# Optimization experiments

Hardware: AMD Instinct MI355X
Metric: run time of the kernel (lower is better)

Reference implementation:

```python
import jax, jax.numpy as jnp
import numpy as np

N = 50000   # nodes
E = 1000000 # edges
D = 64      # input_nf = output_nf = hidden_nf
COORDS_WEIGHT = 1.0


def setup_inputs() -> dict:
    key = jax.random.key(0)
    ks = jax.random.split(key, 16)
    h = jax.random.normal(ks[0], (N, D), dtype=jnp.float32)
    coord = jax.random.normal(ks[1], (N, 3), dtype=jnp.float32)
    edge_index = jax.random.randint(ks[2], (2, E), 0, N, dtype=jnp.int32)
    s = 0.05  # generic init scale
    # edge_mlp: Linear(2D+1 -> D), ReLU, Linear(D -> D), ReLU
    We1 = jax.random.normal(ks[3], (2 * D + 1, D), dtype=jnp.float32) * s
    be1 = jnp.zeros((D,), dtype=jnp.float32)
    We2 = jax.random.normal(ks[4], (D, D), dtype=jnp.float32) * s
    be2 = jnp.zeros((D,), dtype=jnp.float32)
    # node_mlp: Linear(2D -> D), ReLU, Linear(D -> D)
    Wn1 = jax.random.normal(ks[5], (2 * D, D), dtype=jnp.float32) * s
    bn1 = jnp.zeros((D,), dtype=jnp.float32)
    Wn2 = jax.random.normal(ks[6], (D, D), dtype=jnp.float32) * s
    bn2 = jnp.zeros((D,), dtype=jnp.float32)
    # coord_mlp: Linear(D -> D), ReLU, Linear(D -> 1, no bias, xavier gain 0.001)
    Wc1 = jax.random.normal(ks[7], (D, D), dtype=jnp.float32) * s
    bc1 = jnp.zeros((D,), dtype=jnp.float32)
    Wc2 = jax.random.normal(ks[8], (D, 1), dtype=jnp.float32) * 0.001
    return {"h": h, "coord": coord, "edge_index": edge_index,
            "We1": We1, "be1": be1, "We2": We2, "be2": be2,
            "Wn1": Wn1, "bn1": bn1, "Wn2": Wn2, "bn2": bn2,
            "Wc1": Wc1, "bc1": bc1, "Wc2": Wc2}


def reference(h, coord, edge_index, We1, be1, We2, be2, Wn1, bn1, Wn2, bn2, Wc1, bc1, Wc2):
    row, col = edge_index[0], edge_index[1]
    # coord2radial (no PBC offsets; plain pairwise difference)
    coord_diff = coord[row] - coord[col]                    # [E, 3]
    radial = jnp.sum(coord_diff ** 2, axis=1, keepdims=True)  # [E, 1]

    # edge model: MLP on [h_i, h_j, ||x_i - x_j||^2]
    e_in = jnp.concatenate([h[row], h[col], radial], axis=1)  # [E, 2D+1]
    m = jax.nn.relu(e_in @ We1 + be1)
    edge_feat = jax.nn.relu(m @ We2 + be2)                   # [E, D]

    # coord model: per-edge scalar gate, clamp, segment mean
    gate = jax.nn.relu(edge_feat @ Wc1 + bc1) @ Wc2          # [E, 1]
    trans = jnp.clip(coord_diff * gate, -100.0, 100.0)       # [E, 3]
    trans_sum = jax.ops.segment_sum(trans, row, num_segments=N)  # [N, 3]
    cnt = jax.ops.segment_sum(jnp.ones((row.shape[0],), dtype=trans.dtype), row, num_segments=N)
    coord_out = (trans_sum / jnp.maximum(cnt, 1.0)[:, None]) * COORDS_WEIGHT  # [N, 3]

    # node model: scatter-sum aggregate then MLP with residual
    agg = jax.ops.segment_sum(edge_feat, row, num_segments=N)  # [N, D]
    n_in = jnp.concatenate([h, agg], axis=1)                   # [N, 2D]
    h_out = h + (jax.nn.relu(n_in @ Wn1 + bn1) @ Wn2 + bn2)    # residual
    return (h_out, coord_out)
```

## Files before the change

kernel.cpp:

```cpp
#include <hip/hip_runtime.h>

typedef float  f32x4  __attribute__((ext_vector_type(4)));
typedef __bf16 bf16x8 __attribute__((ext_vector_type(8)));
typedef unsigned short u16x8 __attribute__((ext_vector_type(8)));

__device__ inline unsigned short f2b(float f) {
    unsigned u = __builtin_bit_cast(unsigned, f);
    u += 0x7fffu + ((u >> 16) & 1u);
    return (unsigned short)(u >> 16);
}

__device__ inline f32x4 mfma16(bf16x8 a, bf16x8 b, f32x4 c) {
    return __builtin_amdgcn_mfma_f32_16x16x32_bf16(a, b, c, 0, 0, 0);
}

__device__ inline bf16x8 cvt8(f32x4 a, f32x4 b) {
    u16x8 v;
    v[0] = f2b(a[0]); v[1] = f2b(a[1]); v[2] = f2b(a[2]); v[3] = f2b(a[3]);
    v[4] = f2b(b[0]); v[5] = f2b(b[1]); v[6] = f2b(b[2]); v[7] = f2b(b[3]);
    return __builtin_bit_cast(bf16x8, v);
}

__device__ inline bf16x8 ldsA(const unsigned short* base, int frag, int lane) {
    return __builtin_bit_cast(bf16x8,
        *reinterpret_cast<const u16x8*>(base + ((frag * 64 + lane) << 3)));
}

__device__ inline void atom_pk(unsigned short* p, unsigned d) {
    asm volatile("global_atomic_pk_add_bf16 %0, %1, off" :: "v"(p), "v"(d) : "memory");
}

template<bool PK>
__global__ __launch_bounds__(512, 4) void egcl_edge(
    const float* __restrict__ h, const unsigned short* __restrict__ hb,
    const float* __restrict__ coord,
    const int* __restrict__ erow, const int* __restrict__ ecol,
    const float* __restrict__ We1, const float* __restrict__ be1,
    const float* __restrict__ We2, const float* __restrict__ be2,
    const float* __restrict__ Wc1, const float* __restrict__ bc1,
    const float* __restrict__ Wc2,
    float* __restrict__ aggf, unsigned short* __restrict__ aggb,
    float* __restrict__ cacc, int E)
{
    __shared__ __align__(16) unsigned short A1[16 * 512];
    __shared__ __align__(16) unsigned short A2[8 * 512];
    __shared__ __align__(16) unsigned short A3[8 * 512];
    __shared__ __align__(16) float bv[5][64];
    __shared__ __align__(16) unsigned stl[8][16 * 33];

    const int t = threadIdx.x;
    for (int i = t; i < 8192; i += 512) {
        int j = i & 7, lane = (i >> 3) & 63, fi = i >> 9;
        int mt = fi >> 2, ks = fi & 3;
        int in_ch = ks * 32 + ((lane >> 4) << 3) + j;
        int out   = mt * 16 + (lane & 15);
        A1[i] = f2b(We1[in_ch * 64 + out]);
    }
    for (int i = t; i < 4096; i += 512) {
        int j = i & 7, lane = (i >> 3) & 63, fi = i >> 9;
        int mt = fi >> 1, ks = fi & 1;
        int c   = (ks * 2 + (j >> 2)) * 16 + ((lane >> 4) & 3) * 4 + (j & 3);
        int out = mt * 16 + (lane & 15);
        A2[i] = f2b(We2[c * 64 + out]);
        A3[i] = f2b(Wc1[c * 64 + out]);
    }
    if (t < 64) {
        bv[0][t] = be1[t]; bv[1][t] = We1[128 * 64 + t];
        bv[2][t] = be2[t]; bv[3][t] = bc1[t]; bv[4][t] = Wc2[t];
    }
    __syncthreads();

    const int lane = t & 63;
    const int l16 = lane & 15, lq = lane >> 4;
    const int stride = gridDim.x * 8;
    const int wid = (blockIdx.x << 3) + (t >> 6);
    const int ntile = E >> 4;
    const int last = ntile - 1;
    unsigned* st = stl[t >> 6];

    int tile = wid;
    if (tile >= ntile) return;

    if constexpr (PK) {
        int eC = (tile << 4) + l16;
        int rC = erow[eC], cC = ecol[eC];
        u16x8 hr0, hr1, hc0, hc1;
        {
            const u16x8* hr = reinterpret_cast<const u16x8*>(hb + (size_t)rC * 64);
            const u16x8* hc = reinterpret_cast<const u16x8*>(hb + (size_t)cC * 64);
            hr0 = hr[lq]; hr1 = hr[4 + lq]; hc0 = hc[lq]; hc1 = hc[4 + lq];
        }
        float px = 0.f, py = 0.f, pz = 0.f;
        if (lq < 2) {
            int node = (lq == 0) ? rC : cC;
            const float* pp = coord + (size_t)node * 3;
            px = pp[0]; py = pp[1]; pz = pp[2];
        }
        int t1 = tile + stride;
        int tn = (t1 < ntile) ? t1 : last;
        int eN = (tn << 4) + l16;
        int rN = erow[eN], cN = ecol[eN];

        for (; tile < ntile; ) {
            u16x8 nr0, nr1, nc0, nc1;
            {
                const u16x8* hr = reinterpret_cast<const u16x8*>(hb + (size_t)rN * 64);
                const u16x8* hc = reinterpret_cast<const u16x8*>(hb + (size_t)cN * 64);
                nr0 = hr[lq]; nr1 = hr[4 + lq]; nc0 = hc[lq]; nc1 = hc[4 + lq];
            }
            float npx = 0.f, npy = 0.f, npz = 0.f;
            if (lq < 2) {
                int node = (lq == 0) ? rN : cN;
                const float* pp = coord + (size_t)node * 3;
                npx = pp[0]; npy = pp[1]; npz = pp[2];
            }
            int t2 = tile + 2 * stride;
            int t2c = (t2 < ntile) ? t2 : last;
            int e2 = (t2c << 4) + l16;
            int rNN = erow[e2], cNN = ecol[e2];

            float prx = __shfl(px, l16, 64), pry = __shfl(py, l16, 64), prz = __shfl(pz, l16, 64);
            float pcx = __shfl(px, 16 + l16, 64), pcy = __shfl(py, 16 + l16, 64), pcz = __shfl(pz, 16 + l16, 64);
            float dx = prx - pcx, dy = pry - pcy, dz = prz - pcz;
            float rad = dx * dx + dy * dy + dz * dz;

            bf16x8 bR[2] = { __builtin_bit_cast(bf16x8, hr0), __builtin_bit_cast(bf16x8, hr1) };
            bf16x8 bC[2] = { __builtin_bit_cast(bf16x8, hc0), __builtin_bit_cast(bf16x8, hc1) };

            f32x4 a1[4];
#pragma unroll
            for (int mt = 0; mt < 4; ++mt)
                a1[mt] = *reinterpret_cast<const f32x4*>(&bv[0][mt * 16 + lq * 4]);
#pragma unroll
            for (int ks = 0; ks < 2; ++ks)
#pragma unroll
                for (int mt = 0; mt < 4; ++mt)
                    a1[mt] = mfma16(ldsA(A1, mt * 4 + ks, lane), bR[ks], a1[mt]);
#pragma unroll
            for (int ks = 0; ks < 2; ++ks)
#pragma unroll
                for (int mt = 0; mt < 4; ++mt)
                    a1[mt] = mfma16(ldsA(A1, mt * 4 + 2 + ks, lane), bC[ks], a1[mt]);
#pragma unroll
            for (int mt = 0; mt < 4; ++mt) {
                f32x4 w = *reinterpret_cast<const f32x4*>(&bv[1][mt * 16 + lq * 4]);
#pragma unroll
                for (int rr = 0; rr < 4; ++rr)
                    a1[mt][rr] = fmaxf(a1[mt][rr] + rad * w[rr], 0.f);
            }

            bf16x8 b2[2] = { cvt8(a1[0], a1[1]), cvt8(a1[2], a1[3]) };
            f32x4 a2[4];
#pragma unroll
            for (int mt = 0; mt < 4; ++mt)
                a2[mt] = *reinterpret_cast<const f32x4*>(&bv[2][mt * 16 + lq * 4]);
#pragma unroll
            for (int ks = 0; ks < 2; ++ks)
#pragma unroll
                for (int mt = 0; mt < 4; ++mt)
                    a2[mt] = mfma16(ldsA(A2, mt * 2 + ks, lane), b2[ks], a2[mt]);
#pragma unroll
            for (int mt = 0; mt < 4; ++mt)
#pragma unroll
                for (int rr = 0; rr < 4; ++rr)
                    a2[mt][rr] = fmaxf(a2[mt][rr], 0.f);

#pragma unroll
            for (int mt = 0; mt < 4; ++mt) {
                unsigned w0 = (unsigned)f2b(a2[mt][0]) | ((unsigned)f2b(a2[mt][1]) << 16);
                unsigned w1 = (unsigned)f2b(a2[mt][2]) | ((unsigned)f2b(a2[mt][3]) << 16);
                st[l16 * 33 + mt * 8 + lq * 2 + 0] = w0;
                st[l16 * 33 + mt * 8 + lq * 2 + 1] = w1;
            }

            bf16x8 b3[2] = { cvt8(a2[0], a2[1]), cvt8(a2[2], a2[3]) };
            f32x4 a3[4];
#pragma unroll
            for (int mt = 0; mt < 4; ++mt)
                a3[mt] = *reinterpret_cast<const f32x4*>(&bv[3][mt * 16 + lq * 4]);
#pragma unroll
            for (int ks = 0; ks < 2; ++ks)
#pragma unroll
                for (int mt = 0; mt < 4; ++mt)
                    a3[mt] = mfma16(ldsA(A3, mt * 2 + ks, lane), b3[ks], a3[mt]);
            float g = 0.f;
#pragma unroll
            for (int mt = 0; mt < 4; ++mt) {
                f32x4 w = *reinterpret_cast<const f32x4*>(&bv[4][mt * 16 + lq * 4]);
#pragma unroll
                for (int rr = 0; rr < 4; ++rr)
                    g += fmaxf(a3[mt][rr], 0.f) * w[rr];
            }
            g += __shfl_xor(g, 16, 64);
            g += __shfl_xor(g, 32, 64);

#pragma unroll
            for (int i = 0; i < 8; ++i) {
                int e  = (i << 1) | (lane >> 5);
                int cp = ((lane >> 4) & 1) * 16 + (lane & 15);
                unsigned pkd = st[e * 33 + cp];
                int rw = __shfl(rC, e, 64);
                atom_pk(aggb + (size_t)rw * 64 + cp * 2, pkd);
            }

            float dsel = (lq == 0) ? dx : (lq == 1) ? dy : dz;
            float val  = (lq == 3) ? 1.0f : fminf(fmaxf(dsel * g, -100.f), 100.f);
            atomicAdd(&cacc[(size_t)rC * 4 + lq], val);

            tile = t1; t1 = tile + stride;
            rC = rN; cC = cN; rN = rNN; cN = cNN;
            hr0 = nr0; hr1 = nr1; hc0 = nc0; hc1 = nc1;
            px = npx; py = npy; pz = npz;
        }
    } else {
        for (; tile < ntile; tile += stride) {
            const int e = (tile << 4) + l16;
            const int r = erow[e], c = ecol[e];
            const float* pr = coord + (size_t)r * 3;
            const float* pc = coord + (size_t)c * 3;
            float dx = pr[0] - pc[0], dy = pr[1] - pc[1], dz = pr[2] - pc[2];
            float rad = dx * dx + dy * dy + dz * dz;
            const f32x4* hr = reinterpret_cast<const f32x4*>(h + (size_t)r * 64);
            const f32x4* hc = reinterpret_cast<const f32x4*>(h + (size_t)c * 64);
            bf16x8 bR[2], bC[2];
#pragma unroll
            for (int ks = 0; ks < 2; ++ks) {
                bR[ks] = cvt8(hr[ks * 8 + lq * 2], hr[ks * 8 + lq * 2 + 1]);
                bC[ks] = cvt8(hc[ks * 8 + lq * 2], hc[ks * 8 + lq * 2 + 1]);
            }
            f32x4 a1[4];
#pragma unroll
            for (int mt = 0; mt < 4; ++mt)
                a1[mt] = *reinterpret_cast<const f32x4*>(&bv[0][mt * 16 + lq * 4]);
#pragma unroll
            for (int ks = 0; ks < 2; ++ks)
#pragma unroll
                for (int mt = 0; mt < 4; ++mt)
                    a1[mt] = mfma16(ldsA(A1, mt * 4 + ks, lane), bR[ks], a1[mt]);
#pragma unroll
            for (int ks = 0; ks < 2; ++ks)
#pragma unroll
                for (int mt = 0; mt < 4; ++mt)
                    a1[mt] = mfma16(ldsA(A1, mt * 4 + 2 + ks, lane), bC[ks], a1[mt]);
#pragma unroll
            for (int mt = 0; mt < 4; ++mt) {
                f32x4 w = *reinterpret_cast<const f32x4*>(&bv[1][mt * 16 + lq * 4]);
#pragma unroll
                for (int rr = 0; rr < 4; ++rr)
                    a1[mt][rr] = fmaxf(a1[mt][rr] + rad * w[rr], 0.f);
            }
            bf16x8 b2[2] = { cvt8(a1[0], a1[1]), cvt8(a1[2], a1[3]) };
            f32x4 a2[4];
#pragma unroll
            for (int mt = 0; mt < 4; ++mt)
                a2[mt] = *reinterpret_cast<const f32x4*>(&bv[2][mt * 16 + lq * 4]);
#pragma unroll
            for (int ks = 0; ks < 2; ++ks)
#pragma unroll
                for (int mt = 0; mt < 4; ++mt)
                    a2[mt] = mfma16(ldsA(A2, mt * 2 + ks, lane), b2[ks], a2[mt]);
#pragma unroll
            for (int mt = 0; mt < 4; ++mt)
#pragma unroll
                for (int rr = 0; rr < 4; ++rr) {
                    a2[mt][rr] = fmaxf(a2[mt][rr], 0.f);
                    atomicAdd(&aggf[(size_t)r * 64 + mt * 16 + lq * 4 + rr], a2[mt][rr]);
                }
            bf16x8 b3[2] = { cvt8(a2[0], a2[1]), cvt8(a2[2], a2[3]) };
            f32x4 a3[4];
#pragma unroll
            for (int mt = 0; mt < 4; ++mt)
                a3[mt] = *reinterpret_cast<const f32x4*>(&bv[3][mt * 16 + lq * 4]);
#pragma unroll
            for (int ks = 0; ks < 2; ++ks)
#pragma unroll
                for (int mt = 0; mt < 4; ++mt)
                    a3[mt] = mfma16(ldsA(A3, mt * 2 + ks, lane), b3[ks], a3[mt]);
            float g = 0.f;
#pragma unroll
            for (int mt = 0; mt < 4; ++mt) {
                f32x4 w = *reinterpret_cast<const f32x4*>(&bv[4][mt * 16 + lq * 4]);
#pragma unroll
                for (int rr = 0; rr < 4; ++rr)
                    g += fmaxf(a3[mt][rr], 0.f) * w[rr];
            }
            g += __shfl_xor(g, 16, 64);
            g += __shfl_xor(g, 32, 64);
            float dsel = (lq == 0) ? dx : (lq == 1) ? dy : dz;
            float val  = (lq == 3) ? 1.0f : fminf(fmaxf(dsel * g, -100.f), 100.f);
            atomicAdd(&cacc[(size_t)r * 4 + lq], val);
        }
    }
}

__device__ inline void stage_wblock(unsigned short* dst, const float* src, int t, int nthr) {
    for (int i = t; i < 4096; i += nthr) {
        int k = i >> 6, n = i & 63;
        int pos = (((n >> 4) * 2 + (k >> 5)) * 64 + ((((k >> 3) & 3) << 4) | (n & 15))) * 8 + (k & 7);
        dst[pos] = f2b(src[i]);
    }
}

__device__ inline bf16x8 ldsB(const unsigned short* base, int nt, int ks, int lane) {
    return __builtin_bit_cast(bf16x8,
        *reinterpret_cast<const u16x8*>(base + (((nt * 2 + ks) * 64 + lane) << 3)));
}

template<bool PK>
__global__ __launch_bounds__(256) void egcl_node(
    const float* __restrict__ h, const unsigned short* __restrict__ hb,
    const float* __restrict__ aggf, const unsigned short* __restrict__ aggb,
    const float* __restrict__ Wn1, const float* __restrict__ bn1,
    const float* __restrict__ Wn2, const float* __restrict__ bn2,
    float* __restrict__ hout, int N)
{
    __shared__ __align__(16) unsigned short wlds[3][4096];
    __shared__ __align__(16) unsigned short mlds[4][16 * 72];
    __shared__ float bn1l[64], bn2l[64];

    const int t = threadIdx.x;
    stage_wblock(wlds[0], Wn1, t, 256);
    stage_wblock(wlds[1], Wn1 + 64 * 64, t, 256);
    stage_wblock(wlds[2], Wn2, t, 256);
    if (t < 64) { bn1l[t] = bn1[t]; bn2l[t] = bn2[t]; }
    __syncthreads();

    const int wave = t >> 6, lane = t & 63;
    const int l16 = lane & 15, lq = lane >> 4;
    const int ntile = N >> 4;
    unsigned short* ml = mlds[wave];

    for (int tile = blockIdx.x * 4 + wave; tile < ntile; tile += gridDim.x * 4) {
        const int nb = tile << 4;
        bf16x8 fH[2], fA[2];
        if constexpr (PK) {
            const u16x8* ph = reinterpret_cast<const u16x8*>(hb + (size_t)(nb + l16) * 64);
            const u16x8* pa = reinterpret_cast<const u16x8*>(aggb + (size_t)(nb + l16) * 64);
#pragma unroll
            for (int ks = 0; ks < 2; ++ks) {
                fH[ks] = __builtin_bit_cast(bf16x8, ph[ks * 4 + lq]);
                fA[ks] = __builtin_bit_cast(bf16x8, pa[ks * 4 + lq]);
            }
        } else {
            const f32x4* ph = reinterpret_cast<const f32x4*>(h + (size_t)(nb + l16) * 64);
            const f32x4* pa = reinterpret_cast<const f32x4*>(aggf + (size_t)(nb + l16) * 64);
#pragma unroll
            for (int ks = 0; ks < 2; ++ks) {
                fH[ks] = cvt8(ph[ks * 8 + lq * 2], ph[ks * 8 + lq * 2 + 1]);
                fA[ks] = cvt8(pa[ks * 8 + lq * 2], pa[ks * 8 + lq * 2 + 1]);
            }
        }
        f32x4 acc[4];
#pragma unroll
        for (int nt = 0; nt < 4; ++nt) { float b = bn1l[nt * 16 + l16]; acc[nt] = (f32x4){b, b, b, b}; }
#pragma unroll
        for (int ks = 0; ks < 2; ++ks)
#pragma unroll
            for (int nt = 0; nt < 4; ++nt)
                acc[nt] = mfma16(fH[ks], ldsB(wlds[0], nt, ks, lane), acc[nt]);
#pragma unroll
        for (int ks = 0; ks < 2; ++ks)
#pragma unroll
            for (int nt = 0; nt < 4; ++nt)
                acc[nt] = mfma16(fA[ks], ldsB(wlds[1], nt, ks, lane), acc[nt]);
#pragma unroll
        for (int nt = 0; nt < 4; ++nt)
#pragma unroll
            for (int r = 0; r < 4; ++r)
                ml[(lq * 4 + r) * 72 + nt * 16 + l16] = f2b(fmaxf(acc[nt][r], 0.f));
        bf16x8 fM[2];
#pragma unroll
        for (int ks = 0; ks < 2; ++ks)
            fM[ks] = __builtin_bit_cast(bf16x8,
                *reinterpret_cast<const u16x8*>(ml + l16 * 72 + ks * 32 + lq * 8));
        f32x4 acc2[4];
#pragma unroll
        for (int nt = 0; nt < 4; ++nt) { float b = bn2l[nt * 16 + l16]; acc2[nt] = (f32x4){b, b, b, b}; }
#pragma unroll
        for (int ks = 0; ks < 2; ++ks)
#pragma unroll
            for (int nt = 0; nt < 4; ++nt)
                acc2[nt] = mfma16(fM[ks], ldsB(wlds[2], nt, ks, lane), acc2[nt]);
#pragma unroll
        for (int nt = 0; nt < 4; ++nt)
#pragma unroll
            for (int r = 0; r < 4; ++r) {
                size_t idx = (size_t)(nb + lq * 4 + r) * 64 + nt * 16 + l16;
                hout[idx] = h[idx] + acc2[nt][r];
            }
    }
}

__global__ void f32_to_bf16(const float* __restrict__ src, unsigned short* __restrict__ dst, int n8)
{
    int i = blockIdx.x * 256 + threadIdx.x;
    if (i < n8) {
        const f32x4* p = reinterpret_cast<const f32x4*>(src + (size_t)i * 8);
        bf16x8 v = cvt8(p[0], p[1]);
        reinterpret_cast<u16x8*>(dst)[i] = __builtin_bit_cast(u16x8, v);
    }
}

__global__ void egcl_coord(const float* __restrict__ cacc, float* __restrict__ cout, int N)
{
    int n = blockIdx.x * 256 + threadIdx.x;
    if (n < N) {
        f32x4 c = *reinterpret_cast<const f32x4*>(cacc + (size_t)n * 4);
        float inv = 1.f / fmaxf(c[3], 1.f);
        cout[n * 3 + 0] = c[0] * inv;
        cout[n * 3 + 1] = c[1] * inv;
        cout[n * 3 + 2] = c[2] * inv;
    }
}

extern "C" void kernel_launch(void* const* d_in, const int* in_sizes, int n_in,
                              void* d_out, int out_size, void* d_ws, size_t ws_size,
                              hipStream_t stream)
{
    const float* h     = (const float*)d_in[0];
    const float* coord = (const float*)d_in[1];
    const int*   eidx  = (const int*)d_in[2];
    const float* We1 = (const float*)d_in[3];  const float* be1 = (const float*)d_in[4];
    const float* We2 = (const float*)d_in[5];  const float* be2 = (const float*)d_in[6];
    const float* Wn1 = (const float*)d_in[7];  const float* bn1 = (const float*)d_in[8];
    const float* Wn2 = (const float*)d_in[9];  const float* bn2 = (const float*)d_in[10];
    const float* Wc1 = (const float*)d_in[11]; const float* bc1 = (const float*)d_in[12];
    const float* Wc2 = (const float*)d_in[13];

    const int N = in_sizes[0] / 64;
    const int E = in_sizes[2] / 2;

    float* hout = (float*)d_out;
    float* cout = hout + (size_t)N * 64;

    float*          cacc = (float*)d_ws;
    unsigned short* aggb = (unsigned short*)((char*)d_ws + (1u << 20));
    unsigned short* hb   = (unsigned short*)((char*)d_ws + (8u << 20));
    const size_t need = (8u << 20) + (size_t)N * 64 * 2;
    const bool pk = (ws_size >= need);

    hipMemsetAsync(cacc, 0, (size_t)N * 4 * sizeof(float), stream);

    const int ntileN = N >> 4;
    const int nblkN  = (ntileN + 3) / 4;

    if (pk) {
        hipMemsetAsync(aggb, 0, (size_t)N * 64 * 2, stream);
        int n8 = N * 8;
        f32_to_bf16<<<(n8 + 255) / 256, 256, 0, stream>>>(h, hb, n8);
        egcl_edge<true><<<2048, 512, 0, stream>>>(h, hb, coord, eidx, eidx + E,
                                                  We1, be1, We2, be2, Wc1, bc1, Wc2,
                                                  nullptr, aggb, cacc, E);
        egcl_node<true><<<nblkN, 256, 0, stream>>>(h, hb, nullptr, aggb,
                                                   Wn1, bn1, Wn2, bn2, hout, N);
    } else {
        float* aggf = hout;
        hipMemsetAsync(aggf, 0, (size_t)N * 64 * sizeof(float), stream);
        egcl_edge<false><<<2048, 512, 0, stream>>>(h, nullptr, coord, eidx, eidx + E,
                                                   We1, be1, We2, be2, Wc1, bc1, Wc2,
                                                   aggf, nullptr, cacc, E);
        egcl_node<false><<<nblkN, 256, 0, stream>>>(h, nullptr, aggf, nullptr,
                                                    Wn1, bn1, Wn2, bn2, hout, N);
    }
    egcl_coord<<<(N + 255) / 256, 256, 0, stream>>>(cacc, cout, N);
}
```

Before: 203.8 us.

## Sort edges by row into CSR and aggregate per node without atomics

Each call now builds a CSR layout from the edge rows with a histogram, a single-block scan and an atomic scatter. The edge MLP then runs per group of 8 destination nodes, reading the row features once from LDS. Edge messages and coordinate updates are reduced serially within the wave and written directly, which removes the packed bf16 and fp32 global atomics, the memsets and the separate coord-normalisation kernel. In exchange it adds three preprocessing kernels with their own atomics, a serial per-edge flush loop with shuffles, and load imbalance when node degrees vary.

```diff
diff --git a/kernel.cpp b/kernel.cpp
--- a/kernel.cpp
+++ b/kernel.cpp
@@ -26,27 +26,77 @@
         *reinterpret_cast<const u16x8*>(base + ((frag * 64 + lane) << 3)));
 }
 
-__device__ inline void atom_pk(unsigned short* p, unsigned d) {
-    asm volatile("global_atomic_pk_add_bf16 %0, %1, off" :: "v"(p), "v"(d) : "memory");
-}
-
-template<bool PK>
-__global__ __launch_bounds__(512, 4) void egcl_edge(
-    const float* __restrict__ h, const unsigned short* __restrict__ hb,
+__global__ void k_hist(const int* __restrict__ erow, int* __restrict__ cnt, int E)
+{
+    int i = blockIdx.x * 256 + threadIdx.x;
+    if (i < E) atomicAdd(&cnt[erow[i]], 1);
+}
+
+__global__ void k_scan(const int* __restrict__ cnt, int* __restrict__ off,
+                       int* __restrict__ woff, int N, int E)
+{
+    __shared__ int wsum[16];
+    const int t = threadIdx.x;
+    const int lane = t & 63, w = t >> 6;
+    const int chunk = (N + 1023) >> 10;
+    const int lo = t * chunk;
+    const int hi = (lo + chunk < N) ? lo + chunk : N;
+    int s = 0;
+    for (int i = lo; i < hi; ++i) s += cnt[i];
+    int sc = s;
+#pragma unroll
+    for (int d = 1; d < 64; d <<= 1) {
+        int v = __shfl_up(sc, d, 64);
+        if (lane >= d) sc += v;
+    }
+    if (lane == 63) wsum[w] = sc;
+    __syncthreads();
+    if (w == 0 && lane < 16) {
+        int v = wsum[lane];
+        int scw = v;
+#pragma unroll
+        for (int d = 1; d < 16; d <<= 1) {
+            int u = __shfl_up(scw, d, 16);
+            if (lane >= d) scw += u;
+        }
+        wsum[lane] = scw - v;
+    }
+    __syncthreads();
+    int run = wsum[w] + (sc - s);
+    for (int i = lo; i < hi; ++i) {
+        off[i] = run; woff[i] = run;
+        run += cnt[i];
+    }
+    if (t == 0) off[N] = E;
+}
+
+__global__ void k_scatter(const int* __restrict__ erow, const int* __restrict__ ecol,
+                          int* __restrict__ woff, int* __restrict__ scol, int E)
+{
+    int i = blockIdx.x * 256 + threadIdx.x;
+    if (i < E) {
+        int pos = atomicAdd(&woff[erow[i]], 1);
+        scol[pos] = ecol[i];
+    }
+}
+
+__global__ __launch_bounds__(512, 4) void egcl_edge_sorted(
+    const unsigned short* __restrict__ hb,
     const float* __restrict__ coord,
-    const int* __restrict__ erow, const int* __restrict__ ecol,
+    const int* __restrict__ off, const int* __restrict__ scol,
     const float* __restrict__ We1, const float* __restrict__ be1,
     const float* __restrict__ We2, const float* __restrict__ be2,
     const float* __restrict__ Wc1, const float* __restrict__ bc1,
     const float* __restrict__ Wc2,
-    float* __restrict__ aggf, unsigned short* __restrict__ aggb,
-    float* __restrict__ cacc, int E)
+    float* __restrict__ aggf, float* __restrict__ cout, int N)
 {
     __shared__ __align__(16) unsigned short A1[16 * 512];
     __shared__ __align__(16) unsigned short A2[8 * 512];
     __shared__ __align__(16) unsigned short A3[8 * 512];
     __shared__ __align__(16) float bv[5][64];
     __shared__ __align__(16) unsigned stl[8][16 * 33];
+    __shared__ __align__(16) unsigned short hl[8][8 * 72];
+    __shared__ __align__(16) float cl[8][32];
 
     const int t = threadIdx.x;
     for (int i = t; i < 8192; i += 512) {
@@ -72,224 +122,313 @@
 
     const int lane = t & 63;
     const int l16 = lane & 15, lq = lane >> 4;
+    const int w = t >> 6;
+    unsigned* st = stl[w];
+    unsigned short* hrw = hl[w];
+    float* crw = cl[w];
+
+    const int nT = N >> 3;
+    const int tile = blockIdx.x * 8 + w;
+    if (tile >= nT) return;
+    const int nb = tile << 3;
+
+    {
+        int row = lane >> 3, ck = lane & 7;
+        *reinterpret_cast<u16x8*>(hrw + row * 72 + ck * 8) =
+            *reinterpret_cast<const u16x8*>(hb + (size_t)(nb + row) * 64 + ck * 8);
+    }
+    if (lane < 32) {
+        int nn = lane >> 2, c4 = lane & 3;
+        crw[lane] = (c4 < 3) ? coord[(size_t)(nb + nn) * 3 + c4] : 0.f;
+    }
+
+    int ok[9];
+#pragma unroll
+    for (int k = 0; k < 9; ++k) ok[k] = off[nb + k];
+    const int s0 = ok[0], s1 = ok[8];
+    const int dd0 = ok[1]-ok[0], dd1 = ok[2]-ok[1], dd2 = ok[3]-ok[2], dd3 = ok[4]-ok[3];
+    const int dd4 = ok[5]-ok[4], dd5 = ok[6]-ok[5], dd6 = ok[7]-ok[6], dd7 = ok[8]-ok[7];
+
+    int cur = -1; float accv = 0.f, caccv = 0.f;
+    auto FLUSH = [&]() {
+        if (cur >= 0) {
+            aggf[(size_t)(nb + cur) * 64 + lane] = accv;
+            if (lane < 3) {
+                int cc = cur==0?dd0:cur==1?dd1:cur==2?dd2:cur==3?dd3:
+                         cur==4?dd4:cur==5?dd5:cur==6?dd6:dd7;
+                cout[(size_t)(nb + cur) * 3 + lane] = caccv * (1.f / fmaxf((float)cc, 1.f));
+            }
+        }
+    };
+
+    const int nE = s1 - s0;
+    if (nE > 0) {
+        const int s1m1 = s1 - 1;
+        const int nG = (nE + 15) >> 4;
+
+        int gb = s0;
+        int p  = gb + l16;
+        {
+            int pm = (p < s1m1) ? p : s1m1;
+            int c0 = scol[pm];
+            const u16x8* hp = reinterpret_cast<const u16x8*>(hb + (size_t)c0 * 64);
+            u16x8 h0 = hp[lq], h1 = hp[4 + lq];
+            float cx = 0.f, cy = 0.f, cz = 0.f;
+            if (lq == 1) { const float* pp = coord + (size_t)c0 * 3; cx = pp[0]; cy = pp[1]; cz = pp[2]; }
+            int q1 = gb + 16 + l16;
+            int c1 = scol[(q1 < s1m1) ? q1 : s1m1];
+
+            u16x8 hc0 = h0, hc1 = h1;
+            float cpx = cx, cpy = cy, cpz = cz;
+
+            for (int g = 0; g < nG; ++g) {
+                u16x8 nh0, nh1;
+                {
+                    const u16x8* np = reinterpret_cast<const u16x8*>(hb + (size_t)c1 * 64);
+                    nh0 = np[lq]; nh1 = np[4 + lq];
+                }
+                float nx = 0.f, ny = 0.f, nz = 0.f;
+                if (lq == 1) { const float* pp = coord + (size_t)c1 * 3; nx = pp[0]; ny = pp[1]; nz = pp[2]; }
+                int q2 = gb + 32 + l16;
+                int c2 = scol[(q2 < s1m1) ? q2 : s1m1];
+
+                int ni = 0;
+#pragma unroll
+                for (int k = 1; k < 8; ++k) ni += (p >= ok[k]) ? 1 : 0;
+
+                bf16x8 bR[2];
+                bR[0] = __builtin_bit_cast(bf16x8,
+                        *reinterpret_cast<const u16x8*>(hrw + ni * 72 + lq * 8));
+                bR[1] = __builtin_bit_cast(bf16x8,
+                        *reinterpret_cast<const u16x8*>(hrw + ni * 72 + (4 + lq) * 8));
+                bf16x8 bC[2] = { __builtin_bit_cast(bf16x8, hc0), __builtin_bit_cast(bf16x8, hc1) };
+
+                float prx = crw[ni * 4 + 0], pry = crw[ni * 4 + 1], prz = crw[ni * 4 + 2];
+                float pcx = __shfl(cpx, 16 + l16, 64);
+                float pcy = __shfl(cpy, 16 + l16, 64);
+                float pcz = __shfl(cpz, 16 + l16, 64);
+                float dx = prx - pcx, dy = pry - pcy, dz = prz - pcz;
+                float rad = dx * dx + dy * dy + dz * dz;
+
+                f32x4 a1[4];
+#pragma unroll
+                for (int mt = 0; mt < 4; ++mt)
+                    a1[mt] = *reinterpret_cast<const f32x4*>(&bv[0][mt * 16 + lq * 4]);
+#pragma unroll
+                for (int ks = 0; ks < 2; ++ks)
+#pragma unroll
+                    for (int mt = 0; mt < 4; ++mt)
+                        a1[mt] = mfma16(ldsA(A1, mt * 4 + ks, lane), bR[ks], a1[mt]);
+#pragma unroll
+                for (int ks = 0; ks < 2; ++ks)
+#pragma unroll
+                    for (int mt = 0; mt < 4; ++mt)
+                        a1[mt] = mfma16(ldsA(A1, mt * 4 + 2 + ks, lane), bC[ks], a1[mt]);
+#pragma unroll
+                for (int mt = 0; mt < 4; ++mt) {
+                    f32x4 wv = *reinterpret_cast<const f32x4*>(&bv[1][mt * 16 + lq * 4]);
+#pragma unroll
+                    for (int rr = 0; rr < 4; ++rr)
+                        a1[mt][rr] = fmaxf(a1[mt][rr] + rad * wv[rr], 0.f);
+                }
+
+                bf16x8 b2[2] = { cvt8(a1[0], a1[1]), cvt8(a1[2], a1[3]) };
+                f32x4 a2[4];
+#pragma unroll
+                for (int mt = 0; mt < 4; ++mt)
+                    a2[mt] = *reinterpret_cast<const f32x4*>(&bv[2][mt * 16 + lq * 4]);
+#pragma unroll
+                for (int ks = 0; ks < 2; ++ks)
+#pragma unroll
+                    for (int mt = 0; mt < 4; ++mt)
+                        a2[mt] = mfma16(ldsA(A2, mt * 2 + ks, lane), b2[ks], a2[mt]);
+#pragma unroll
+                for (int mt = 0; mt < 4; ++mt)
+#pragma unroll
+                    for (int rr = 0; rr < 4; ++rr)
+                        a2[mt][rr] = fmaxf(a2[mt][rr], 0.f);
+
+#pragma unroll
+                for (int mt = 0; mt < 4; ++mt) {
+                    unsigned w0 = (unsigned)f2b(a2[mt][0]) | ((unsigned)f2b(a2[mt][1]) << 16);
+                    unsigned w1 = (unsigned)f2b(a2[mt][2]) | ((unsigned)f2b(a2[mt][3]) << 16);
+                    st[l16 * 33 + mt * 8 + lq * 2 + 0] = w0;
+                    st[l16 * 33 + mt * 8 + lq * 2 + 1] = w1;
+                }
+
+                bf16x8 b3[2] = { cvt8(a2[0], a2[1]), cvt8(a2[2], a2[3]) };
+                f32x4 a3[4];
+#pragma unroll
+                for (int mt = 0; mt < 4; ++mt)
+                    a3[mt] = *reinterpret_cast<const f32x4*>(&bv[3][mt * 16 + lq * 4]);
+#pragma unroll
+                for (int ks = 0; ks < 2; ++ks)
+#pragma unroll
+                    for (int mt = 0; mt < 4; ++mt)
+                        a3[mt] = mfma16(ldsA(A3, mt * 2 + ks, lane), b3[ks], a3[mt]);
+                float gg = 0.f;
+#pragma unroll
+                for (int mt = 0; mt < 4; ++mt) {
+                    f32x4 wv = *reinterpret_cast<const f32x4*>(&bv[4][mt * 16 + lq * 4]);
+#pragma unroll
+                    for (int rr = 0; rr < 4; ++rr)
+                        gg += fmaxf(a3[mt][rr], 0.f) * wv[rr];
+                }
+                gg += __shfl_xor(gg, 16, 64);
+                gg += __shfl_xor(gg, 32, 64);
+
+                float dsel = (lq == 0) ? dx : (lq == 1) ? dy : dz;
+                float val  = fminf(fmaxf(dsel * gg, -100.f), 100.f);
+
+#pragma unroll
+                for (int e = 0; e < 16; ++e) {
+                    if (gb + e < s1) {
+                        int nv = __shfl(ni, e, 64);
+                        unsigned wrd = st[e * 33 + (lane >> 1)];
+                        float v = __builtin_bit_cast(float,
+                                  (lane & 1) ? (wrd & 0xffff0000u) : (wrd << 16));
+                        float cv = __shfl(val, ((lane & 3) << 4) + e, 64);
+                        if (nv != cur) { FLUSH(); cur = nv; accv = v; caccv = cv; }
+                        else           { accv += v; caccv += cv; }
+                    }
+                }
+
+                gb += 16; p += 16;
+                c1 = c2;
+                hc0 = nh0; hc1 = nh1;
+                cpx = nx; cpy = ny; cpz = nz;
+            }
+        }
+        FLUSH();
+    }
+
+#pragma unroll
+    for (int k = 0; k < 8; ++k) {
+        if (ok[k + 1] == ok[k]) {
+            aggf[(size_t)(nb + k) * 64 + lane] = 0.f;
+            if (lane < 3) cout[(size_t)(nb + k) * 3 + lane] = 0.f;
+        }
+    }
+}
+
+__global__ __launch_bounds__(512, 4) void egcl_edge_fb(
+    const float* __restrict__ h, const float* __restrict__ coord,
+    const int* __restrict__ erow, const int* __restrict__ ecol,
+    const float* __restrict__ We1, const float* __restrict__ be1,
+    const float* __restrict__ We2, const float* __restrict__ be2,
+    const float* __restrict__ Wc1, const float* __restrict__ bc1,
+    const float* __restrict__ Wc2,
+    float* __restrict__ aggf, float* __restrict__ cacc, int E)
+{
+    __shared__ __align__(16) unsigned short A1[16 * 512];
+    __shared__ __align__(16) unsigned short A2[8 * 512];
+    __shared__ __align__(16) unsigned short A3[8 * 512];
+    __shared__ __align__(16) float bv[5][64];
+
+    const int t = threadIdx.x;
+    for (int i = t; i < 8192; i += 512) {
+        int j = i & 7, lane = (i >> 3) & 63, fi = i >> 9;
+        int mt = fi >> 2, ks = fi & 3;
+        int in_ch = ks * 32 + ((lane >> 4) << 3) + j;
+        int out   = mt * 16 + (lane & 15);
+        A1[i] = f2b(We1[in_ch * 64 + out]);
+    }
+    for (int i = t; i < 4096; i += 512) {
+        int j = i & 7, lane = (i >> 3) & 63, fi = i >> 9;
+        int mt = fi >> 1, ks = fi & 1;
+        int c   = (ks * 2 + (j >> 2)) * 16 + ((lane >> 4) & 3) * 4 + (j & 3);
+        int out = mt * 16 + (lane & 15);
+        A2[i] = f2b(We2[c * 64 + out]);
+        A3[i] = f2b(Wc1[c * 64 + out]);
+    }
+    if (t < 64) {
+        bv[0][t] = be1[t]; bv[1][t] = We1[128 * 64 + t];
+        bv[2][t] = be2[t]; bv[3][t] = bc1[t]; bv[4][t] = Wc2[t];
+    }
+    __syncthreads();
+
+    const int lane = t & 63;
+    const int l16 = lane & 15, lq = lane >> 4;
     const int stride = gridDim.x * 8;
     const int wid = (blockIdx.x << 3) + (t >> 6);
     const int ntile = E >> 4;
-    const int last = ntile - 1;
-    unsigned* st = stl[t >> 6];
-
-    int tile = wid;
-    if (tile >= ntile) return;
-
-    if constexpr (PK) {
-        int eC = (tile << 4) + l16;
-        int rC = erow[eC], cC = ecol[eC];
-        u16x8 hr0, hr1, hc0, hc1;
-        {
-            const u16x8* hr = reinterpret_cast<const u16x8*>(hb + (size_t)rC * 64);
-            const u16x8* hc = reinterpret_cast<const u16x8*>(hb + (size_t)cC * 64);
-            hr0 = hr[lq]; hr1 = hr[4 + lq]; hc0 = hc[lq]; hc1 = hc[4 + lq];
-        }
-        float px = 0.f, py = 0.f, pz = 0.f;
-        if (lq < 2) {
-            int node = (lq == 0) ? rC : cC;
-            const float* pp = coord + (size_t)node * 3;
-            px = pp[0]; py = pp[1]; pz = pp[2];
-        }
-        int t1 = tile + stride;
-        int tn = (t1 < ntile) ? t1 : last;
-        int eN = (tn << 4) + l16;
-        int rN = erow[eN], cN = ecol[eN];
-
-        for (; tile < ntile; ) {
-            u16x8 nr0, nr1, nc0, nc1;
-            {
-                const u16x8* hr = reinterpret_cast<const u16x8*>(hb + (size_t)rN * 64);
-                const u16x8* hc = reinterpret_cast<const u16x8*>(hb + (size_t)cN * 64);
-                nr0 = hr[lq]; nr1 = hr[4 + lq]; nc0 = hc[lq]; nc1 = hc[4 + lq];
+
+    for (int tile = wid; tile < ntile; tile += stride) {
+        const int e = (tile << 4) + l16;
+        const int r = erow[e], c = ecol[e];
+        const float* pr = coord + (size_t)r * 3;
+        const float* pc = coord + (size_t)c * 3;
+        float dx = pr[0] - pc[0], dy = pr[1] - pc[1], dz = pr[2] - pc[2];
+        float rad = dx * dx + dy * dy + dz * dz;
+        const f32x4* hr = reinterpret_cast<const f32x4*>(h + (size_t)r * 64);
+        const f32x4* hc = reinterpret_cast<const f32x4*>(h + (size_t)c * 64);
+        bf16x8 bR[2], bC[2];
+#pragma unroll
+        for (int ks = 0; ks < 2; ++ks) {
+            bR[ks] = cvt8(hr[ks * 8 + lq * 2], hr[ks * 8 + lq * 2 + 1]);
+            bC[ks] = cvt8(hc[ks * 8 + lq * 2], hc[ks * 8 + lq * 2 + 1]);
+        }
+        f32x4 a1[4];
+#pragma unroll
+        for (int mt = 0; mt < 4; ++mt)
+            a1[mt] = *reinterpret_cast<const f32x4*>(&bv[0][mt * 16 + lq * 4]);
+#pragma unroll
+        for (int ks = 0; ks < 2; ++ks)
+#pragma unroll
+            for (int mt = 0; mt < 4; ++mt)
+                a1[mt] = mfma16(ldsA(A1, mt * 4 + ks, lane), bR[ks], a1[mt]);
+#pragma unroll
+        for (int ks = 0; ks < 2; ++ks)
+#pragma unroll
+            for (int mt = 0; mt < 4; ++mt)
+                a1[mt] = mfma16(ldsA(A1, mt * 4 + 2 + ks, lane), bC[ks], a1[mt]);
+#pragma unroll
+        for (int mt = 0; mt < 4; ++mt) {
+            f32x4 wv = *reinterpret_cast<const f32x4*>(&bv[1][mt * 16 + lq * 4]);
+#pragma unroll
+            for (int rr = 0; rr < 4; ++rr)
+                a1[mt][rr] = fmaxf(a1[mt][rr] + rad * wv[rr], 0.f);
+        }
+        bf16x8 b2[2] = { cvt8(a1[0], a1[1]), cvt8(a1[2], a1[3]) };
+        f32x4 a2[4];
+#pragma unroll
+        for (int mt = 0; mt < 4; ++mt)
+            a2[mt] = *reinterpret_cast<const f32x4*>(&bv[2][mt * 16 + lq * 4]);
+#pragma unroll
+        for (int ks = 0; ks < 2; ++ks)
+#pragma unroll
+            for (int mt = 0; mt < 4; ++mt)
+                a2[mt] = mfma16(ldsA(A2, mt * 2 + ks, lane), b2[ks], a2[mt]);
+#pragma unroll
+        for (int mt = 0; mt < 4; ++mt)
+#pragma unroll
+            for (int rr = 0; rr < 4; ++rr) {
+                a2[mt][rr] = fmaxf(a2[mt][rr], 0.f);
+                atomicAdd(&aggf[(size_t)r * 64 + mt * 16 + lq * 4 + rr], a2[mt][rr]);
             }
-            float npx = 0.f, npy = 0.f, npz = 0.f;
-            if (lq < 2) {
-                int node = (lq == 0) ? rN : cN;
-                const float* pp = coord + (size_t)node * 3;
-                npx = pp[0]; npy = pp[1]; npz = pp[2];
-            }
-            int t2 = tile + 2 * stride;
-            int t2c = (t2 < ntile) ? t2 : last;
-            int e2 = (t2c << 4) + l16;
-            int rNN = erow[e2], cNN = ecol[e2];
-
-            float prx = __shfl(px, l16, 64), pry = __shfl(py, l16, 64), prz = __shfl(pz, l16, 64);
-            float pcx = __shfl(px, 16 + l16, 64), pcy = __shfl(py, 16 + l16, 64), pcz = __shfl(pz, 16 + l16, 64);
-            float dx = prx - pcx, dy = pry - pcy, dz = prz - pcz;
-            float rad = dx * dx + dy * dy + dz * dz;
-
-            bf16x8 bR[2] = { __builtin_bit_cast(bf16x8, hr0), __builtin_bit_cast(bf16x8, hr1) };
-            bf16x8 bC[2] = { __builtin_bit_cast(bf16x8, hc0), __builtin_bit_cast(bf16x8, hc1) };
-
-            f32x4 a1[4];
+        bf16x8 b3[2] = { cvt8(a2[0], a2[1]), cvt8(a2[2], a2[3]) };
+        f32x4 a3[4];
+#pragma unroll
+        for (int mt = 0; mt < 4; ++mt)
+            a3[mt] = *reinterpret_cast<const f32x4*>(&bv[3][mt * 16 + lq * 4]);
+#pragma unroll
+        for (int ks = 0; ks < 2; ++ks)
 #pragma unroll
             for (int mt = 0; mt < 4; ++mt)
-                a1[mt] = *reinterpret_cast<const f32x4*>(&bv[0][mt * 16 + lq * 4]);
-#pragma unroll
-            for (int ks = 0; ks < 2; ++ks)
-#pragma unroll
-                for (int mt = 0; mt < 4; ++mt)
-                    a1[mt] = mfma16(ldsA(A1, mt * 4 + ks, lane), bR[ks], a1[mt]);
-#pragma unroll
-            for (int ks = 0; ks < 2; ++ks)
-#pragma unroll
-                for (int mt = 0; mt < 4; ++mt)
-                    a1[mt] = mfma16(ldsA(A1, mt * 4 + 2 + ks, lane), bC[ks], a1[mt]);
-#pragma unroll
-            for (int mt = 0; mt < 4; ++mt) {
-                f32x4 w = *reinterpret_cast<const f32x4*>(&bv[1][mt * 16 + lq * 4]);
-#pragma unroll
-                for (int rr = 0; rr < 4; ++rr)
-                    a1[mt][rr] = fmaxf(a1[mt][rr] + rad * w[rr], 0.f);
-            }
-
-            bf16x8 b2[2] = { cvt8(a1[0], a1[1]), cvt8(a1[2], a1[3]) };
-            f32x4 a2[4];
-#pragma unroll
-            for (int mt = 0; mt < 4; ++mt)
-                a2[mt] = *reinterpret_cast<const f32x4*>(&bv[2][mt * 16 + lq * 4]);
-#pragma unroll
-            for (int ks = 0; ks < 2; ++ks)
-#pragma unroll
-                for (int mt = 0; mt < 4; ++mt)
-                    a2[mt] = mfma16(ldsA(A2, mt * 2 + ks, lane), b2[ks], a2[mt]);
-#pragma unroll
-            for (int mt = 0; mt < 4; ++mt)
-#pragma unroll
-                for (int rr = 0; rr < 4; ++rr)
-                    a2[mt][rr] = fmaxf(a2[mt][rr], 0.f);
-
-#pragma unroll
-            for (int mt = 0; mt < 4; ++mt) {
-                unsigned w0 = (unsigned)f2b(a2[mt][0]) | ((unsigned)f2b(a2[mt][1]) << 16);
-                unsigned w1 = (unsigned)f2b(a2[mt][2]) | ((unsigned)f2b(a2[mt][3]) << 16);
-                st[l16 * 33 + mt * 8 + lq * 2 + 0] = w0;
-                st[l16 * 33 + mt * 8 + lq * 2 + 1] = w1;
-            }
-
-            bf16x8 b3[2] = { cvt8(a2[0], a2[1]), cvt8(a2[2], a2[3]) };
-            f32x4 a3[4];
-#pragma unroll
-            for (int mt = 0; mt < 4; ++mt)
-                a3[mt] = *reinterpret_cast<const f32x4*>(&bv[3][mt * 16 + lq * 4]);
-#pragma unroll
-            for (int ks = 0; ks < 2; ++ks)
-#pragma unroll
-                for (int mt = 0; mt < 4; ++mt)
-                    a3[mt] = mfma16(ldsA(A3, mt * 2 + ks, lane), b3[ks], a3[mt]);
-            float g = 0.f;
-#pragma unroll
-            for (int mt = 0; mt < 4; ++mt) {
-                f32x4 w = *reinterpret_cast<const f32x4*>(&bv[4][mt * 16 + lq * 4]);
-#pragma unroll
-                for (int rr = 0; rr < 4; ++rr)
-                    g += fmaxf(a3[mt][rr], 0.f) * w[rr];
-            }
-            g += __shfl_xor(g, 16, 64);
-            g += __shfl_xor(g, 32, 64);
-
-#pragma unroll
-            for (int i = 0; i < 8; ++i) {
-                int e  = (i << 1) | (lane >> 5);
-                int cp = ((lane >> 4) & 1) * 16 + (lane & 15);
-                unsigned pkd = st[e * 33 + cp];
-                int rw = __shfl(rC, e, 64);
-                atom_pk(aggb + (size_t)rw * 64 + cp * 2, pkd);
-            }
-
-            float dsel = (lq == 0) ? dx : (lq == 1) ? dy : dz;
-            float val  = (lq == 3) ? 1.0f : fminf(fmaxf(dsel * g, -100.f), 100.f);
-            atomicAdd(&cacc[(size_t)rC * 4 + lq], val);
-
-            tile = t1; t1 = tile + stride;
-            rC = rN; cC = cN; rN = rNN; cN = cNN;
-            hr0 = nr0; hr1 = nr1; hc0 = nc0; hc1 = nc1;
-            px = npx; py = npy; pz = npz;
-        }
-    } else {
-        for (; tile < ntile; tile += stride) {
-            const int e = (tile << 4) + l16;
-            const int r = erow[e], c = ecol[e];
-            const float* pr = coord + (size_t)r * 3;
-            const float* pc = coord + (size_t)c * 3;
-            float dx = pr[0] - pc[0], dy = pr[1] - pc[1], dz = pr[2] - pc[2];
-            float rad = dx * dx + dy * dy + dz * dz;
-            const f32x4* hr = reinterpret_cast<const f32x4*>(h + (size_t)r * 64);
-            const f32x4* hc = reinterpret_cast<const f32x4*>(h + (size_t)c * 64);
-            bf16x8 bR[2], bC[2];
-#pragma unroll
-            for (int ks = 0; ks < 2; ++ks) {
-                bR[ks] = cvt8(hr[ks * 8 + lq * 2], hr[ks * 8 + lq * 2 + 1]);
-                bC[ks] = cvt8(hc[ks * 8 + lq * 2], hc[ks * 8 + lq * 2 + 1]);
-            }
-            f32x4 a1[4];
-#pragma unroll
-            for (int mt = 0; mt < 4; ++mt)
-                a1[mt] = *reinterpret_cast<const f32x4*>(&bv[0][mt * 16 + lq * 4]);
-#pragma unroll
-            for (int ks = 0; ks < 2; ++ks)
-#pragma unroll
-                for (int mt = 0; mt < 4; ++mt)
-                    a1[mt] = mfma16(ldsA(A1, mt * 4 + ks, lane), bR[ks], a1[mt]);
-#pragma unroll
-            for (int ks = 0; ks < 2; ++ks)
-#pragma unroll
-                for (int mt = 0; mt < 4; ++mt)
-                    a1[mt] = mfma16(ldsA(A1, mt * 4 + 2 + ks, lane), bC[ks], a1[mt]);
-#pragma unroll
-            for (int mt = 0; mt < 4; ++mt) {
-                f32x4 w = *reinterpret_cast<const f32x4*>(&bv[1][mt * 16 + lq * 4]);
-#pragma unroll
-                for (int rr = 0; rr < 4; ++rr)
-                    a1[mt][rr] = fmaxf(a1[mt][rr] + rad * w[rr], 0.f);
-            }
-            bf16x8 b2[2] = { cvt8(a1[0], a1[1]), cvt8(a1[2], a1[3]) };
-            f32x4 a2[4];
-#pragma unroll
-            for (int mt = 0; mt < 4; ++mt)
-                a2[mt] = *reinterpret_cast<const f32x4*>(&bv[2][mt * 16 + lq * 4]);
-#pragma unroll
-            for (int ks = 0; ks < 2; ++ks)
-#pragma unroll
-                for (int mt = 0; mt < 4; ++mt)
-                    a2[mt] = mfma16(ldsA(A2, mt * 2 + ks, lane), b2[ks], a2[mt]);
-#pragma unroll
-            for (int mt = 0; mt < 4; ++mt)
-#pragma unroll
-                for (int rr = 0; rr < 4; ++rr) {
-                    a2[mt][rr] = fmaxf(a2[mt][rr], 0.f);
-                    atomicAdd(&aggf[(size_t)r * 64 + mt * 16 + lq * 4 + rr], a2[mt][rr]);
-                }
-            bf16x8 b3[2] = { cvt8(a2[0], a2[1]), cvt8(a2[2], a2[3]) };
-            f32x4 a3[4];
-#pragma unroll
-            for (int mt = 0; mt < 4; ++mt)
-                a3[mt] = *reinterpret_cast<const f32x4*>(&bv[3][mt * 16 + lq * 4]);
-#pragma unroll
-            for (int ks = 0; ks < 2; ++ks)
-#pragma unroll
-                for (int mt = 0; mt < 4; ++mt)
-                    a3[mt] = mfma16(ldsA(A3, mt * 2 + ks, lane), b3[ks], a3[mt]);
-            float g = 0.f;
-#pragma unroll
-            for (int mt = 0; mt < 4; ++mt) {
-                f32x4 w = *reinterpret_cast<const f32x4*>(&bv[4][mt * 16 + lq * 4]);
-#pragma unroll
-                for (int rr = 0; rr < 4; ++rr)
-                    g += fmaxf(a3[mt][rr], 0.f) * w[rr];
-            }
-            g += __shfl_xor(g, 16, 64);
-            g += __shfl_xor(g, 32, 64);
-            float dsel = (lq == 0) ? dx : (lq == 1) ? dy : dz;
-            float val  = (lq == 3) ? 1.0f : fminf(fmaxf(dsel * g, -100.f), 100.f);
-            atomicAdd(&cacc[(size_t)r * 4 + lq], val);
-        }
+                a3[mt] = mfma16(ldsA(A3, mt * 2 + ks, lane), b3[ks], a3[mt]);
+        float gg = 0.f;
+#pragma unroll
+        for (int mt = 0; mt < 4; ++mt) {
+            f32x4 wv = *reinterpret_cast<const f32x4*>(&bv[4][mt * 16 + lq * 4]);
+#pragma unroll
+            for (int rr = 0; rr < 4; ++rr)
+                gg += fmaxf(a3[mt][rr], 0.f) * wv[rr];
+        }
+        gg += __shfl_xor(gg, 16, 64);
+        gg += __shfl_xor(gg, 32, 64);
+        float dsel = (lq == 0) ? dx : (lq == 1) ? dy : dz;
+        float val  = (lq == 3) ? 1.0f : fminf(fmaxf(dsel * gg, -100.f), 100.f);
+        atomicAdd(&cacc[(size_t)r * 4 + lq], val);
     }
 }
 
@@ -306,10 +445,8 @@
         *reinterpret_cast<const u16x8*>(base + (((nt * 2 + ks) * 64 + lane) << 3)));
 }
 
-template<bool PK>
-__global__ __launch_bounds__(256) void egcl_node(
-    const float* __restrict__ h, const unsigned short* __restrict__ hb,
-    const float* __restrict__ aggf, const unsigned short* __restrict__ aggb,
+__global__ __launch_bounds__(256) void egcl_node_fb(
+    const float* __restrict__ h, const float* __restrict__ aggf,
     const float* __restrict__ Wn1, const float* __restrict__ bn1,
     const float* __restrict__ Wn2, const float* __restrict__ bn2,
     float* __restrict__ hout, int N)
@@ -333,22 +470,12 @@
     for (int tile = blockIdx.x * 4 + wave; tile < ntile; tile += gridDim.x * 4) {
         const int nb = tile << 4;
         bf16x8 fH[2], fA[2];
-        if constexpr (PK) {
-            const u16x8* ph = reinterpret_cast<const u16x8*>(hb + (size_t)(nb + l16) * 64);
-            const u16x8* pa = reinterpret_cast<const u16x8*>(aggb + (size_t)(nb + l16) * 64);
-#pragma unroll
-            for (int ks = 0; ks < 2; ++ks) {
-                fH[ks] = __builtin_bit_cast(bf16x8, ph[ks * 4 + lq]);
-                fA[ks] = __builtin_bit_cast(bf16x8, pa[ks * 4 + lq]);
-            }
-        } else {
-            const f32x4* ph = reinterpret_cast<const f32x4*>(h + (size_t)(nb + l16) * 64);
-            const f32x4* pa = reinterpret_cast<const f32x4*>(aggf + (size_t)(nb + l16) * 64);
-#pragma unroll
-            for (int ks = 0; ks < 2; ++ks) {
-                fH[ks] = cvt8(ph[ks * 8 + lq * 2], ph[ks * 8 + lq * 2 + 1]);
-                fA[ks] = cvt8(pa[ks * 8 + lq * 2], pa[ks * 8 + lq * 2 + 1]);
-            }
+        const f32x4* ph = reinterpret_cast<const f32x4*>(h + (size_t)(nb + l16) * 64);
+        const f32x4* pa = reinterpret_cast<const f32x4*>(aggf + (size_t)(nb + l16) * 64);
+#pragma unroll
+        for (int ks = 0; ks < 2; ++ks) {
+            fH[ks] = cvt8(ph[ks * 8 + lq * 2], ph[ks * 8 + lq * 2 + 1]);
+            fA[ks] = cvt8(pa[ks * 8 + lq * 2], pa[ks * 8 + lq * 2 + 1]);
         }
         f32x4 acc[4];
 #pragma unroll
@@ -433,34 +560,41 @@
     float* hout = (float*)d_out;
     float* cout = hout + (size_t)N * 64;
 
-    float*          cacc = (float*)d_ws;
-    unsigned short* aggb = (unsigned short*)((char*)d_ws + (1u << 20));
-    unsigned short* hb   = (unsigned short*)((char*)d_ws + (8u << 20));
-    const size_t need = (8u << 20) + (size_t)N * 64 * 2;
-    const bool pk = (ws_size >= need);
-
-    hipMemsetAsync(cacc, 0, (size_t)N * 4 * sizeof(float), stream);
-
     const int ntileN = N >> 4;
     const int nblkN  = (ntileN + 3) / 4;
 
-    if (pk) {
-        hipMemsetAsync(aggb, 0, (size_t)N * 64 * 2, stream);
+    int* cnt  = (int*)d_ws;
+    int* off  = (int*)((char*)d_ws + (256u << 10));
+    int* woff = (int*)((char*)d_ws + (512u << 10));
+    int* scol = (int*)((char*)d_ws + (1u << 20));
+    unsigned short* hb = (unsigned short*)((char*)d_ws + (5u << 20));
+
+    const size_t need_sorted = (5u << 20) + (size_t)N * 128;
+    const bool use_sorted = (ws_size >= need_sorted) && (N % 16 == 0) && N > 0
+                            && ((size_t)E * 4 <= (4u << 20));
+
+    if (use_sorted) {
+        hipMemsetAsync(cnt, 0, (size_t)N * sizeof(int), stream);
         int n8 = N * 8;
         f32_to_bf16<<<(n8 + 255) / 256, 256, 0, stream>>>(h, hb, n8);
-        egcl_edge<true><<<2048, 512, 0, stream>>>(h, hb, coord, eidx, eidx + E,
-                                                  We1, be1, We2, be2, Wc1, bc1, Wc2,
-                                                  nullptr, aggb, cacc, E);
-        egcl_node<true><<<nblkN, 256, 0, stream>>>(h, hb, nullptr, aggb,
-                                                   Wn1, bn1, Wn2, bn2, hout, N);
+        k_hist<<<(E + 255) / 256, 256, 0, stream>>>(eidx, cnt, E);
+        k_scan<<<1, 1024, 0, stream>>>(cnt, off, woff, N, E);
+        k_scatter<<<(E + 255) / 256, 256, 0, stream>>>(eidx, eidx + E, woff, scol, E);
+        const int nTe = N >> 3;
+        egcl_edge_sorted<<<(nTe + 7) / 8, 512, 0, stream>>>(
+            hb, coord, off, scol, We1, be1, We2, be2, Wc1, bc1, Wc2,
+            hout , cout, N);
+        egcl_node_fb<<<nblkN, 256, 0, stream>>>(h, hout ,
+                                                Wn1, bn1, Wn2, bn2, hout, N);
     } else {
+        float* cacc = (float*)d_ws;
         float* aggf = hout;
+        hipMemsetAsync(cacc, 0, (size_t)N * 4 * sizeof(float), stream);
         hipMemsetAsync(aggf, 0, (size_t)N * 64 * sizeof(float), stream);
-        egcl_edge<false><<<2048, 512, 0, stream>>>(h, nullptr, coord, eidx, eidx + E,
-                                                   We1, be1, We2, be2, Wc1, bc1, Wc2,
-                                                   aggf, nullptr, cacc, E);
-        egcl_node<false><<<nblkN, 256, 0, stream>>>(h, nullptr, aggf, nullptr,
-                                                    Wn1, bn1, Wn2, bn2, hout, N);
-    }
-    egcl_coord<<<(N + 255) / 256, 256, 0, stream>>>(cacc, cout, N);
-}
+        egcl_edge_fb<<<2048, 512, 0, stream>>>(h, coord, eidx, eidx + E,
+                                               We1, be1, We2, be2, Wc1, bc1, Wc2,
+                                               aggf, cacc, E);
+        egcl_node_fb<<<nblkN, 256, 0, stream>>>(h, aggf, Wn1, bn1, Wn2, bn2, hout, N);
+        egcl_coord<<<(N + 255) / 256, 256, 0, stream>>>(cacc, cout, N);
+    }
+}
```

Result: slower. 799.3 us (+292.2%).
